# Kernel optimization log

Measured on AMD Instinct MI355X. Metric: run time of the kernel, lower is better.

## Reference

```python
import jax, jax.numpy as jnp
import numpy as np

N_HEAD = 16

def setup_inputs() -> dict:
    key = jax.random.key(0)
    ks = jax.random.split(key, 9)
    H = 2048
    def w(k, shape, scale=0.02):
        return jax.random.normal(k, shape, dtype=jnp.float32) * scale
    return {
        'h':  jax.random.normal(ks[0], (4, 2048, H), dtype=jnp.float32),
        'Wq': w(ks[1], (H, H)), 'bq': w(ks[2], (H,)),
        'Wk': w(ks[3], (H, H)), 'bk': w(ks[4], (H,)),
        'Wv': w(ks[5], (H, H)), 'bv': w(ks[6], (H,)),
        'Wo': w(ks[7], (H, H)), 'bo': w(ks[8], (H,)),
    }

def reference(h, Wq, bq, Wk, bk, Wv, bv, Wo, bo):
    B, S, H = h.shape
    nh = N_HEAD
    hd = H // nh
    # QKV projections (torch Linear: x @ W.T + b)
    q = (h @ Wq.T + bq).reshape(B, S, nh, hd)
    k = (h @ Wk.T + bk).reshape(B, S, nh, hd)
    v = (h @ Wv.T + bv).reshape(B, S, nh, hd)
    scale = 1.0 / jnp.sqrt(jnp.float32(hd))
    # causal attention scores [B, nh, S, S]
    scores = jnp.einsum('bqhd,bkhd->bhqk', q, k) * scale
    causal = jnp.tril(jnp.ones((S, S), dtype=bool))
    scores = jnp.where(causal, scores, jnp.finfo(scores.dtype).min)
    attn = jax.nn.softmax(scores, axis=-1)
    o = jnp.einsum('bhqk,bkhd->bqhd', attn, v).reshape(B, S, H)
    return o @ Wo.T + bo
```

## Files before the change

kernel.cpp:

```cpp
#include <hip/hip_runtime.h>
#include <hip/hip_bf16.h>
#include <math.h>


using bf16x8 = __attribute__((ext_vector_type(8))) __bf16;
using f32x4  = __attribute__((ext_vector_type(4))) float;
using s16x8  = __attribute__((ext_vector_type(8))) short;

#define MFMA16(a, b, c) __builtin_amdgcn_mfma_f32_16x16x32_bf16((a), (b), (c), 0, 0, 0)

__device__ __forceinline__ unsigned short f2bf(float f) {
  unsigned u = __float_as_uint(f);
  u += 0x7FFFu + ((u >> 16) & 1u);
  return (unsigned short)(u >> 16);
}

__device__ __forceinline__ void gload16(const void* g, void* l) {
  __builtin_amdgcn_global_load_lds((const __attribute__((address_space(1))) void*)g,
                                   (__attribute__((address_space(3))) void*)l,
                                   16, 0, 0);
}

__global__ void cvt_all(const float* __restrict__ h,
                        const float* __restrict__ Wq, const float* __restrict__ Wk,
                        const float* __restrict__ Wv, const float* __restrict__ Wo,
                        unsigned short* __restrict__ h_bf,
                        unsigned short* __restrict__ dqkv,
                        unsigned short* __restrict__ dwo) {
  int i = blockIdx.x * 256 + threadIdx.x;
  const float* s; unsigned short* d; int j;
  if (i < 2097152) {
    s = h; d = h_bf; j = i;
  } else {
    int w = (i - 2097152) >> 19;
    j = i & 524287;
    s = (w == 0) ? Wq : (w == 1) ? Wk : (w == 2) ? Wv : Wo;
    d = (w < 3) ? dqkv + w * 4194304 : dwo;
  }
  float4 v0 = ((const float4*)s)[2 * j];
  float4 v1 = ((const float4*)s)[2 * j + 1];
  s16x8 o;
  o[0] = (short)f2bf(v0.x); o[1] = (short)f2bf(v0.y);
  o[2] = (short)f2bf(v0.z); o[3] = (short)f2bf(v0.w);
  o[4] = (short)f2bf(v1.x); o[5] = (short)f2bf(v1.y);
  o[6] = (short)f2bf(v1.z); o[7] = (short)f2bf(v1.w);
  ((s16x8*)d)[j] = o;
}


#define GEMM_PRE()                                                             \
  const int tid = threadIdx.x;                                                 \
  const int wave = tid >> 6, lane = tid & 63;                                  \
  const int lo = lane & 15, hi = lane >> 4;                                    \
  const int wr = wave >> 2, wc = wave & 3;                                     \
  const int r4 = lane >> 2, s4 = lane & 3;                                     \
  const int scol = ((s4 ^ ((r4 >> 1) & 3)) << 3);                              \
  const unsigned short* aS[2]; const unsigned short* bS[2];                    \
  _Pragma("unroll")                                                            \
  for (int j = 0; j < 2; ++j) {                                                \
    aS[j] = A + (size_t)(m0 + (wave * 2 + j) * 16 + r4) * 2048 + scol;         \
    bS[j] = W + (size_t)(n0 + (wave * 2 + j) * 16 + r4) * 2048 + scol;         \
  }                                                                            \
  f32x4 acc[8][4] = {};

#define STAGE2(BUF, J)                                                         \
  do {                                                                         \
    gload16(aS[J], &lA[BUF][(wave * 2 + (J)) * 512]);                          \
    gload16(bS[J], &lB[BUF][(wave * 2 + (J)) * 512]);                          \
    aS[J] += 32; bS[J] += 32;                                                  \
  } while (0)

#define LDA4_(dst, MH, BUF)                                                    \
  do {                                                                         \
    _Pragma("unroll")                                                          \
    for (int im = 0; im < 4; ++im)                                             \
      dst[im] = *(const bf16x8*)&lA[BUF][(wr * 128 + (MH)*64 + im * 16 + lo) * 32 + \
                                         ((hi ^ ((lo >> 1) & 3)) << 3)];       \
  } while (0)

#define LDB4_(dst, BUF)                                                        \
  do {                                                                         \
    _Pragma("unroll")                                                          \
    for (int ni = 0; ni < 4; ++ni)                                             \
      dst[ni] = *(const bf16x8*)&lB[BUF][(wc * 64 + ni * 16 + lo) * 32 +       \
                                         ((hi ^ ((lo >> 1) & 3)) << 3)];       \
  } while (0)

#define MF16NP(MH, aF, bF)                                                     \
  do {                                                                         \
    _Pragma("unroll")                                                          \
    for (int im = 0; im < 4; ++im)                                             \
      _Pragma("unroll")                                                        \
      for (int ni = 0; ni < 4; ++ni)                                           \
        acc[(MH)*4 + im][ni] = MFMA16(aF[im], bF[ni], acc[(MH)*4 + im][ni]);   \
  } while (0)

#define BAR __builtin_amdgcn_s_barrier()
#define VMC(N) asm volatile("s_waitcnt vmcnt(" #N ")" ::: "memory")

#define TILE(RBUF, SBUF, COND, VN)                                             \
  do {                                                                         \
    bf16x8 aF[4], aG[4], bF[4];                                                \
    LDA4_(aF, 0, RBUF); LDB4_(bF, RBUF); LDA4_(aG, 1, RBUF);                   \
    if (COND) { STAGE2(SBUF, 0); STAGE2(SBUF, 1); }                            \
    __builtin_amdgcn_s_setprio(1);                                             \
    MF16NP(0, aF, bF);                                                         \
    MF16NP(1, aG, bF);                                                         \
    __builtin_amdgcn_s_setprio(0);                                             \
    VMC(VN); BAR;                                                              \
  } while (0)

#define GEMM_MAIN()                                                            \
  STAGE2(0, 0); STAGE2(0, 1); STAGE2(1, 0); STAGE2(1, 1);                      \
  STAGE2(2, 0); STAGE2(2, 1);                                                  \
  VMC(8); BAR;                                                                 \
  for (int u = 0; u < 15; ++u) {                                               \
    TILE(0, 3, true, 8); TILE(1, 0, true, 8);                                  \
    TILE(2, 1, true, 8); TILE(3, 2, true, 8);                                  \
  }                                                                            \
  TILE(0, 3, true, 8); TILE(1, 0, false, 4);                                   \
  TILE(2, 1, false, 0); TILE(3, 2, false, 0);

__global__ __launch_bounds__(512, 2)
void gemm_qkv(const unsigned short* __restrict__ A,
              const unsigned short* __restrict__ W,
              const float* __restrict__ bq, const float* __restrict__ bk,
              const float* __restrict__ bv,
              unsigned short* __restrict__ Q, unsigned short* __restrict__ Kq,
              unsigned short* __restrict__ V) {
  __shared__ unsigned short lA[4][256 * 32];
  __shared__ unsigned short lB[4][256 * 32];
  const int bid = blockIdx.x;
  const int sid = (bid & 7) * 96 + (bid >> 3);
  const int bm = sid / 24, bn = sid % 24;
  const int m0 = bm * 256, n0 = bn * 256;
  GEMM_PRE();
  GEMM_MAIN();

  const int which = n0 >> 11;
  const float* bias = (which == 0) ? bq : (which == 1) ? bk : bv;
  unsigned short* dst = (which == 0) ? Q : (which == 1) ? Kq : V;

  unsigned short* patch = (wave < 4) ? (&lA[0][0] + wave * 4608)
                                     : (&lB[0][0] + (wave - 4) * 4608);
  const int nbase = n0 + wc * 64;
  const int head = (nbase & 2047) >> 7;
  const int d0 = nbase & 127;
#pragma unroll
  for (int pass = 0; pass < 2; ++pass) {
    asm volatile("s_waitcnt lgkmcnt(0)" ::: "memory");
#pragma unroll
    for (int mi = 0; mi < 4; ++mi)
#pragma unroll
      for (int ni = 0; ni < 4; ++ni) {
        int n2 = (nbase + ni * 16 + lo) & 2047;
        float bb = bias[n2];
#pragma unroll
        for (int i = 0; i < 4; ++i)
          patch[(mi * 16 + hi * 4 + i) * 72 + ni * 16 + lo] =
              f2bf(acc[pass * 4 + mi][ni][i] + bb);
      }
    asm volatile("s_waitcnt lgkmcnt(0)" ::: "memory");
#pragma unroll
    for (int it = 0; it < 8; ++it) {
      int rl = it * 8 + (lane >> 3);
      int coff = (lane & 7) * 8;
      s16x8 v = *(const s16x8*)&patch[rl * 72 + coff];
      int m = m0 + wr * 128 + pass * 64 + rl;
      int b = m >> 11, s = m & 2047;
      *(s16x8*)&dst[(((size_t)b * 16 + head) * 2048 + s) * 128 + d0 + coff] = v;
    }
  }
}

__global__ __launch_bounds__(512, 2)
void gemm_out(const unsigned short* __restrict__ A,
              const unsigned short* __restrict__ W,
              const float* __restrict__ bo, float* __restrict__ out) {
  __shared__ unsigned short lA[4][256 * 32];
  __shared__ unsigned short lB[4][256 * 32];
  const int bid = blockIdx.x;
  const int sid = (bid & 7) * 32 + (bid >> 3);
  const int bm = sid >> 3, bn = sid & 7;
  const int m0 = bm * 256, n0 = bn * 256;
  GEMM_PRE();
  GEMM_MAIN();

  float* patch = (float*)((wave < 4) ? (&lA[0][0] + wave * 4352)
                                     : (&lB[0][0] + (wave - 4) * 4352));
  const int nbase = n0 + wc * 64;
#pragma unroll
  for (int pass = 0; pass < 4; ++pass) {
    asm volatile("s_waitcnt lgkmcnt(0)" ::: "memory");
#pragma unroll
    for (int mi = 0; mi < 2; ++mi)
#pragma unroll
      for (int ni = 0; ni < 4; ++ni) {
        float bb = bo[nbase + ni * 16 + lo];
#pragma unroll
        for (int i = 0; i < 4; ++i)
          patch[(mi * 16 + hi * 4 + i) * 68 + ni * 16 + lo] =
              acc[pass * 2 + mi][ni][i] + bb;
      }
    asm volatile("s_waitcnt lgkmcnt(0)" ::: "memory");
#pragma unroll
    for (int it = 0; it < 8; ++it) {
      int rl = it * 4 + hi;
      int coff = lo * 4;
      float4 v = *(const float4*)&patch[rl * 68 + coff];
      int m = m0 + wr * 128 + pass * 32 + rl;
      *(float4*)&out[(size_t)m * 2048 + nbase + coff] = v;
    }
  }
}

__global__ __launch_bounds__(256, 2)
void attn_kernel(const unsigned short* __restrict__ Qb,
                 const unsigned short* __restrict__ Kb,
                 const unsigned short* __restrict__ Vb,
                 unsigned short* __restrict__ Ob) {
  __shared__ unsigned short lK[2][64 * 128];
  __shared__ unsigned short lVt[144 * 72];
  __shared__ unsigned short lP[4][32 * 72];

  const int tid = threadIdx.x;
  const int wave = tid >> 6, lane = tid & 63;
  const int lo = lane & 15, hi = lane >> 4;
  const int bh = blockIdx.x & 63;
  const int pr = blockIdx.x >> 6;
  const size_t base = (size_t)bh * 2048 * 128;
  const float SCL = 0.08838834764831845f * 1.4426950408889634f;
  const float THR = 11.5416f;
  const int rr = tid & 31, c0v = (tid >> 5) * 8;

#pragma unroll
  for (int x = tid; x < 1024; x += 256)
    lVt[(128 + (x >> 6)) * 72 + (x & 63)] = 0x3F80;

#define STAGEK(KT2, BUF)                                                       \
  do {                                                                         \
    _Pragma("unroll")                                                          \
    for (int j = 0; j < 4; j++) {                                              \
      int lrow = j * 16 + wave * 4 + hi;                                       \
      int srccol = (lo * 16) ^ ((lrow & 7) << 4);                              \
      gload16(Kb + base + (size_t)((KT2) * 64 + lrow) * 128 + (srccol >> 1),   \
              &lK[BUF][(j * 16 + wave * 4) * 128]);                            \
    }                                                                          \
  } while (0)

  for (int hseq = 0; hseq < 2; ++hseq) {
    const int qt = hseq ? pr : 15 - pr;
    const int q0 = qt * 128 + wave * 32;
    const int ktn = qt * 2 + 2;
    const int qmax_w = q0 + 31;

    bf16x8 aq[2][4];
#pragma unroll
    for (int mi = 0; mi < 2; mi++)
#pragma unroll
      for (int dk = 0; dk < 4; dk++)
        aq[mi][dk] = *(const bf16x8*)&Qb[base + (size_t)(q0 + mi * 16 + lo) * 128 + dk * 32 + hi * 8];

    f32x4 acc[2][9] = {};
    float mrun[2][4];
#pragma unroll
    for (int a = 0; a < 2; a++)
#pragma unroll
      for (int b = 0; b < 4; b++) mrun[a][b] = -INFINITY;

    STAGEK(0, 0);

    for (int kt = 0; kt < ktn; kt++) {
      const unsigned short* vp0 = Vb + base + (size_t)(kt * 64 + 2 * rr) * 128 + c0v;
      s16x8 v00 = *(const s16x8*)vp0;
      s16x8 v01 = *(const s16x8*)(vp0 + 128);
      s16x8 v10 = *(const s16x8*)(vp0 + 64);
      s16x8 v11 = *(const s16x8*)(vp0 + 192);
      if (kt + 1 < ktn) { STAGEK(kt + 1, (kt + 1) & 1); VMC(8); }
      else { VMC(0); }
      BAR;

      const bool docomp = (kt * 64 <= qmax_w);
      if (docomp) {
        const unsigned short* lKc = &lK[kt & 1][0];
        f32x4 sc[2][4] = {};
        __builtin_amdgcn_s_setprio(1);
#pragma unroll
        for (int ni = 0; ni < 4; ni++)
#pragma unroll
          for (int dk = 0; dk < 4; dk++) {
            int row = ni * 16 + lo;
            int col = (dk * 32 + hi * 8) ^ ((row & 7) << 3);
            bf16x8 bk_ = *(const bf16x8*)&lKc[row * 128 + col];
            sc[0][ni] = MFMA16(aq[0][dk], bk_, sc[0][ni]);
            sc[1][ni] = MFMA16(aq[1][dk], bk_, sc[1][ni]);
          }
        __builtin_amdgcn_s_setprio(0);
        float tm[2][4];
        bool cond = true;
#pragma unroll
        for (int mi = 0; mi < 2; mi++)
#pragma unroll
          for (int i = 0; i < 4; i++) {
            int qrow = q0 + mi * 16 + hi * 4 + i;
            float mx = -INFINITY;
#pragma unroll
            for (int ni = 0; ni < 4; ni++) {
              int kc = kt * 64 + ni * 16 + lo;
              float s = sc[mi][ni][i] * SCL;
              if (kc > qrow) s = -INFINITY;
              sc[mi][ni][i] = s;
              mx = fmaxf(mx, s);
            }
            tm[mi][i] = mx;
            cond = cond && (mx <= mrun[mi][i] + THR);
          }
        if (!__all((int)cond)) {
#pragma unroll
          for (int mi = 0; mi < 2; mi++)
#pragma unroll
            for (int i = 0; i < 4; i++) {
              float mt = tm[mi][i];
              mt = fmaxf(mt, __shfl_xor(mt, 1));
              mt = fmaxf(mt, __shfl_xor(mt, 2));
              mt = fmaxf(mt, __shfl_xor(mt, 4));
              mt = fmaxf(mt, __shfl_xor(mt, 8));
              float mo = mrun[mi][i];
              float mn = fmaxf(mo, mt);
              float alpha = exp2f(mo - mn);
              mrun[mi][i] = mn;
#pragma unroll
              for (int ni = 0; ni < 9; ni++) acc[mi][ni][i] *= alpha;
            }
        }
        unsigned short* lPw = &lP[wave][0];
#pragma unroll
        for (int mi = 0; mi < 2; mi++)
#pragma unroll
          for (int i = 0; i < 4; i++) {
            float m = mrun[mi][i];
            int prow = mi * 16 + hi * 4 + i;
#pragma unroll
            for (int ni = 0; ni < 4; ni++)
              lPw[prow * 72 + ni * 16 + lo] = f2bf(exp2f(sc[mi][ni][i] - m));
          }
      }

#pragma unroll
      for (int j = 0; j < 8; j++) {
        *(ushort2*)&lVt[(c0v + j) * 72 + 2 * rr] =
            make_ushort2((unsigned short)v00[j], (unsigned short)v01[j]);
        *(ushort2*)&lVt[(c0v + 64 + j) * 72 + 2 * rr] =
            make_ushort2((unsigned short)v10[j], (unsigned short)v11[j]);
      }
      asm volatile("s_waitcnt lgkmcnt(0)" ::: "memory");
      BAR;

      if (docomp) {
        unsigned short* lPw = &lP[wave][0];
        bf16x8 ap[2][2];
#pragma unroll
        for (int mi = 0; mi < 2; mi++)
#pragma unroll
          for (int k2 = 0; k2 < 2; k2++)
            ap[mi][k2] = *(const bf16x8*)&lPw[(mi * 16 + lo) * 72 + k2 * 32 + hi * 8];
        __builtin_amdgcn_s_setprio(1);
#pragma unroll
        for (int ni = 0; ni < 9; ni++)
#pragma unroll
          for (int k2 = 0; k2 < 2; k2++) {
            bf16x8 bv_ = *(const bf16x8*)&lVt[(ni * 16 + lo) * 72 + k2 * 32 + hi * 8];
            acc[0][ni] = MFMA16(ap[0][k2], bv_, acc[0][ni]);
            acc[1][ni] = MFMA16(ap[1][k2], bv_, acc[1][ni]);
          }
        __builtin_amdgcn_s_setprio(0);
      }
    }

    const int b = bh >> 4, hh = bh & 15;
#pragma unroll
    for (int mi = 0; mi < 2; mi++)
#pragma unroll
      for (int i = 0; i < 4; i++) {
        float inv = 1.0f / acc[mi][8][i];
        int s = q0 + mi * 16 + hi * 4 + i;
        size_t rowbase = ((size_t)b * 2048 + s) * 2048 + hh * 128 + lo;
#pragma unroll
        for (int ni = 0; ni < 8; ni++)
          Ob[rowbase + ni * 16] = f2bf(acc[mi][ni][i] * inv);
      }
  }
}

extern "C" void kernel_launch(void* const* d_in, const int* in_sizes, int n_in,
                              void* d_out, int out_size, void* d_ws, size_t ws_size,
                              hipStream_t stream) {
  const float* h  = (const float*)d_in[0];
  const float* Wq = (const float*)d_in[1];
  const float* bq = (const float*)d_in[2];
  const float* Wk = (const float*)d_in[3];
  const float* bk = (const float*)d_in[4];
  const float* Wv = (const float*)d_in[5];
  const float* bv = (const float*)d_in[6];
  const float* Wo = (const float*)d_in[7];
  const float* bo = (const float*)d_in[8];
  float* out = (float*)d_out;

  char* ws = (char*)d_ws;
  unsigned short* h_bf  = (unsigned short*)(ws + 0);
  unsigned short* Qb    = (unsigned short*)(ws + 33554432);
  unsigned short* Kb    = (unsigned short*)(ws + 67108864);
  unsigned short* Vb    = (unsigned short*)(ws + 100663296);
  unsigned short* Wqkv  = (unsigned short*)(ws + 134217728);
  unsigned short* Wo_bf = (unsigned short*)(ws + 159383552);
  unsigned short* Ob    = h_bf;

  cvt_all<<<16384, 256, 0, stream>>>(h, Wq, Wk, Wv, Wo, h_bf, Wqkv, Wo_bf);

  gemm_qkv<<<dim3(768), dim3(512), 0, stream>>>(h_bf, Wqkv, bq, bk, bv, Qb, Kb, Vb);

  attn_kernel<<<dim3(512), dim3(256), 0, stream>>>(Qb, Kb, Vb, Ob);

  gemm_out<<<dim3(256), dim3(512), 0, stream>>>(Ob, Wo_bf, bo, out);
}
```

Measured before the change: 420.4 us.

## Shrink GEMM tiles to 256x128 with triple-buffered LDS for higher occupancy

Both projection GEMMs move from 256x256 to 256x128 output tiles and from a 4-deep to a 3-deep LDS ring, which cuts shared memory per block. Launch bounds rise to 4 blocks per CU and grid sizes double. The point is better occupancy and wave count: gemm_out now has 512 blocks instead of 256 on a 256-CU part. The cost is lower arithmetic intensity per tile and more global traffic for A, plus fewer accumulator registers per wave, so the 4-block bound may or may not be met.

```diff
diff --git a/kernel.cpp b/kernel.cpp
--- a/kernel.cpp
+++ b/kernel.cpp
@@ -55,35 +55,33 @@
   const int wr = wave >> 2, wc = wave & 3;                                     \
   const int r4 = lane >> 2, s4 = lane & 3;                                     \
   const int scol = ((s4 ^ ((r4 >> 1) & 3)) << 3);                              \
-  const unsigned short* aS[2]; const unsigned short* bS[2];                    \
+  const int swz = ((hi ^ ((lo >> 1) & 3)) << 3);                               \
+  const unsigned short* aS[2]; const unsigned short* bS;                       \
   _Pragma("unroll")                                                            \
-  for (int j = 0; j < 2; ++j) {                                                \
+  for (int j = 0; j < 2; ++j)                                                  \
     aS[j] = A + (size_t)(m0 + (wave * 2 + j) * 16 + r4) * 2048 + scol;         \
-    bS[j] = W + (size_t)(n0 + (wave * 2 + j) * 16 + r4) * 2048 + scol;         \
-  }                                                                            \
-  f32x4 acc[8][4] = {};
-
-#define STAGE2(BUF, J)                                                         \
-  do {                                                                         \
-    gload16(aS[J], &lA[BUF][(wave * 2 + (J)) * 512]);                          \
-    gload16(bS[J], &lB[BUF][(wave * 2 + (J)) * 512]);                          \
-    aS[J] += 32; bS[J] += 32;                                                  \
+  bS = W + (size_t)(n0 + wave * 16 + r4) * 2048 + scol;                        \
+  f32x4 acc[8][2] = {};
+
+#define STAGE3(BUF)                                                            \
+  do {                                                                         \
+    gload16(aS[0], &lA[BUF][(wave * 2 + 0) * 512]); aS[0] += 32;               \
+    gload16(aS[1], &lA[BUF][(wave * 2 + 1) * 512]); aS[1] += 32;               \
+    gload16(bS, &lB[BUF][wave * 512]); bS += 32;                               \
   } while (0)
 
 #define LDA4_(dst, MH, BUF)                                                    \
   do {                                                                         \
     _Pragma("unroll")                                                          \
     for (int im = 0; im < 4; ++im)                                             \
-      dst[im] = *(const bf16x8*)&lA[BUF][(wr * 128 + (MH)*64 + im * 16 + lo) * 32 + \
-                                         ((hi ^ ((lo >> 1) & 3)) << 3)];       \
-  } while (0)
-
-#define LDB4_(dst, BUF)                                                        \
+      dst[im] = *(const bf16x8*)&lA[BUF][(wr * 128 + (MH)*64 + im * 16 + lo) * 32 + swz]; \
+  } while (0)
+
+#define LDB2_(dst, BUF)                                                        \
   do {                                                                         \
     _Pragma("unroll")                                                          \
-    for (int ni = 0; ni < 4; ++ni)                                             \
-      dst[ni] = *(const bf16x8*)&lB[BUF][(wc * 64 + ni * 16 + lo) * 32 +       \
-                                         ((hi ^ ((lo >> 1) & 3)) << 3)];       \
+    for (int ni = 0; ni < 2; ++ni)                                             \
+      dst[ni] = *(const bf16x8*)&lB[BUF][(wc * 32 + ni * 16 + lo) * 32 + swz]; \
   } while (0)
 
 #define MF16NP(MH, aF, bF)                                                     \
@@ -91,7 +89,7 @@
     _Pragma("unroll")                                                          \
     for (int im = 0; im < 4; ++im)                                             \
       _Pragma("unroll")                                                        \
-      for (int ni = 0; ni < 4; ++ni)                                           \
+      for (int ni = 0; ni < 2; ++ni)                                           \
         acc[(MH)*4 + im][ni] = MFMA16(aF[im], bF[ni], acc[(MH)*4 + im][ni]);   \
   } while (0)
 
@@ -100,9 +98,9 @@
 
 #define TILE(RBUF, SBUF, COND, VN)                                             \
   do {                                                                         \
-    bf16x8 aF[4], aG[4], bF[4];                                                \
-    LDA4_(aF, 0, RBUF); LDB4_(bF, RBUF); LDA4_(aG, 1, RBUF);                   \
-    if (COND) { STAGE2(SBUF, 0); STAGE2(SBUF, 1); }                            \
+    bf16x8 aF[4], aG[4], bF[2];                                                \
+    LDA4_(aF, 0, RBUF); LDB2_(bF, RBUF); LDA4_(aG, 1, RBUF);                   \
+    if (COND) STAGE3(SBUF);                                                    \
     __builtin_amdgcn_s_setprio(1);                                             \
     MF16NP(0, aF, bF);                                                         \
     MF16NP(1, aG, bF);                                                         \
@@ -111,29 +109,27 @@
   } while (0)
 
 #define GEMM_MAIN()                                                            \
-  STAGE2(0, 0); STAGE2(0, 1); STAGE2(1, 0); STAGE2(1, 1);                      \
-  STAGE2(2, 0); STAGE2(2, 1);                                                  \
-  VMC(8); BAR;                                                                 \
-  for (int u = 0; u < 15; ++u) {                                               \
-    TILE(0, 3, true, 8); TILE(1, 0, true, 8);                                  \
-    TILE(2, 1, true, 8); TILE(3, 2, true, 8);                                  \
+  STAGE3(0); STAGE3(1);                                                        \
+  VMC(3); BAR;                                                                 \
+  for (int u = 0; u < 20; ++u) {                                               \
+    TILE(0, 2, true, 3); TILE(1, 0, true, 3); TILE(2, 1, true, 3);             \
   }                                                                            \
-  TILE(0, 3, true, 8); TILE(1, 0, false, 4);                                   \
-  TILE(2, 1, false, 0); TILE(3, 2, false, 0);
-
-__global__ __launch_bounds__(512, 2)
+  TILE(0, 2, true, 3); TILE(1, 0, true, 3);                                    \
+  TILE(2, 1, false, 0); TILE(0, 0, false, 0);
+
+__global__ __launch_bounds__(512, 4)
 void gemm_qkv(const unsigned short* __restrict__ A,
               const unsigned short* __restrict__ W,
               const float* __restrict__ bq, const float* __restrict__ bk,
               const float* __restrict__ bv,
               unsigned short* __restrict__ Q, unsigned short* __restrict__ Kq,
               unsigned short* __restrict__ V) {
-  __shared__ unsigned short lA[4][256 * 32];
-  __shared__ unsigned short lB[4][256 * 32];
+  __shared__ unsigned short lA[3][256 * 32];
+  __shared__ unsigned short lB[3][128 * 32];
   const int bid = blockIdx.x;
-  const int sid = (bid & 7) * 96 + (bid >> 3);
-  const int bm = sid / 24, bn = sid % 24;
-  const int m0 = bm * 256, n0 = bn * 256;
+  const int sid = (bid & 7) * 192 + (bid >> 3);
+  const int bm = sid / 48, bn = sid % 48;
+  const int m0 = bm * 256, n0 = bn * 128;
   GEMM_PRE();
   GEMM_MAIN();
 
@@ -141,31 +137,30 @@
   const float* bias = (which == 0) ? bq : (which == 1) ? bk : bv;
   unsigned short* dst = (which == 0) ? Q : (which == 1) ? Kq : V;
 
-  unsigned short* patch = (wave < 4) ? (&lA[0][0] + wave * 4608)
-                                     : (&lB[0][0] + (wave - 4) * 4608);
-  const int nbase = n0 + wc * 64;
+  unsigned short* patch = &lA[0][0] + wave * 2560;
+  const int nbase = n0 + wc * 32;
   const int head = (nbase & 2047) >> 7;
   const int d0 = nbase & 127;
+  float bb[2];
+#pragma unroll
+  for (int ni = 0; ni < 2; ++ni) bb[ni] = bias[(nbase + ni * 16 + lo) & 2047];
 #pragma unroll
   for (int pass = 0; pass < 2; ++pass) {
     asm volatile("s_waitcnt lgkmcnt(0)" ::: "memory");
 #pragma unroll
     for (int mi = 0; mi < 4; ++mi)
 #pragma unroll
-      for (int ni = 0; ni < 4; ++ni) {
-        int n2 = (nbase + ni * 16 + lo) & 2047;
-        float bb = bias[n2];
+      for (int ni = 0; ni < 2; ++ni)
 #pragma unroll
         for (int i = 0; i < 4; ++i)
-          patch[(mi * 16 + hi * 4 + i) * 72 + ni * 16 + lo] =
-              f2bf(acc[pass * 4 + mi][ni][i] + bb);
-      }
+          patch[(mi * 16 + hi * 4 + i) * 40 + ni * 16 + lo] =
+              f2bf(acc[pass * 4 + mi][ni][i] + bb[ni]);
     asm volatile("s_waitcnt lgkmcnt(0)" ::: "memory");
 #pragma unroll
-    for (int it = 0; it < 8; ++it) {
-      int rl = it * 8 + (lane >> 3);
-      int coff = (lane & 7) * 8;
-      s16x8 v = *(const s16x8*)&patch[rl * 72 + coff];
+    for (int it = 0; it < 4; ++it) {
+      int rl = it * 16 + (lane >> 2);
+      int coff = (lane & 3) * 8;
+      s16x8 v = *(const s16x8*)&patch[rl * 40 + coff];
       int m = m0 + wr * 128 + pass * 64 + rl;
       int b = m >> 11, s = m & 2047;
       *(s16x8*)&dst[(((size_t)b * 16 + head) * 2048 + s) * 128 + d0 + coff] = v;
@@ -173,41 +168,41 @@
   }
 }
 
-__global__ __launch_bounds__(512, 2)
+__global__ __launch_bounds__(512, 4)
 void gemm_out(const unsigned short* __restrict__ A,
               const unsigned short* __restrict__ W,
               const float* __restrict__ bo, float* __restrict__ out) {
-  __shared__ unsigned short lA[4][256 * 32];
-  __shared__ unsigned short lB[4][256 * 32];
+  __shared__ unsigned short lA[3][256 * 32];
+  __shared__ unsigned short lB[3][128 * 32];
   const int bid = blockIdx.x;
-  const int sid = (bid & 7) * 32 + (bid >> 3);
-  const int bm = sid >> 3, bn = sid & 7;
-  const int m0 = bm * 256, n0 = bn * 256;
+  const int sid = (bid & 7) * 64 + (bid >> 3);
+  const int bm = sid >> 4, bn = sid & 15;
+  const int m0 = bm * 256, n0 = bn * 128;
   GEMM_PRE();
   GEMM_MAIN();
 
-  float* patch = (float*)((wave < 4) ? (&lA[0][0] + wave * 4352)
-                                     : (&lB[0][0] + (wave - 4) * 4352));
-  const int nbase = n0 + wc * 64;
+  float* patch = (float*)(&lA[0][0]) + wave * 1152;
+  const int nbase = n0 + wc * 32;
+  float bb[2];
+#pragma unroll
+  for (int ni = 0; ni < 2; ++ni) bb[ni] = bo[nbase + ni * 16 + lo];
 #pragma unroll
   for (int pass = 0; pass < 4; ++pass) {
     asm volatile("s_waitcnt lgkmcnt(0)" ::: "memory");
 #pragma unroll
     for (int mi = 0; mi < 2; ++mi)
 #pragma unroll
-      for (int ni = 0; ni < 4; ++ni) {
-        float bb = bo[nbase + ni * 16 + lo];
+      for (int ni = 0; ni < 2; ++ni)
 #pragma unroll
         for (int i = 0; i < 4; ++i)
-          patch[(mi * 16 + hi * 4 + i) * 68 + ni * 16 + lo] =
-              acc[pass * 2 + mi][ni][i] + bb;
-      }
+          patch[(mi * 16 + hi * 4 + i) * 36 + ni * 16 + lo] =
+              acc[pass * 2 + mi][ni][i] + bb[ni];
     asm volatile("s_waitcnt lgkmcnt(0)" ::: "memory");
 #pragma unroll
-    for (int it = 0; it < 8; ++it) {
-      int rl = it * 4 + hi;
-      int coff = lo * 4;
-      float4 v = *(const float4*)&patch[rl * 68 + coff];
+    for (int it = 0; it < 4; ++it) {
+      int rl = it * 8 + (lane >> 3);
+      int coff = (lane & 7) * 4;
+      float4 v = *(const float4*)&patch[rl * 36 + coff];
       int m = m0 + wr * 128 + pass * 32 + rl;
       *(float4*)&out[(size_t)m * 2048 + nbase + coff] = v;
     }
@@ -417,9 +412,9 @@
 
   cvt_all<<<16384, 256, 0, stream>>>(h, Wq, Wk, Wv, Wo, h_bf, Wqkv, Wo_bf);
 
-  gemm_qkv<<<dim3(768), dim3(512), 0, stream>>>(h_bf, Wqkv, bq, bk, bv, Qb, Kb, Vb);
+  gemm_qkv<<<dim3(1536), dim3(512), 0, stream>>>(h_bf, Wqkv, bq, bk, bv, Qb, Kb, Vb);
 
   attn_kernel<<<dim3(512), dim3(256), 0, stream>>>(Qb, Kb, Vb, Ob);
 
-  gemm_out<<<dim3(256), dim3(512), 0, stream>>>(Ob, Wo_bf, bo, out);
-}
+  gemm_out<<<dim3(512), dim3(512), 0, stream>>>(Ob, Wo_bf, bo, out);
+}
```

After: 459.7 us. 9.3% more time.

## Restructure GEMM main loop into finer-grained A/B staged ping-pong windows

Applied to the files above, without the earlier changes.

Replaces the 4-buffer, one-tile-per-barrier GEMM pipeline with a 2x2 LDS layout. Each 128-wide K window is split into eight half-tile MFMA phases separated by barriers. Global-to-LDS loads for A and B are issued separately and interleaved with the phases, which aims to overlap memory traffic with MFMA work at finer granularity. In exchange there are many more barriers per K step, and the waitcnt accounting must stay correct.

```diff
diff --git a/kernel.cpp b/kernel.cpp
--- a/kernel.cpp
+++ b/kernel.cpp
@@ -55,71 +55,104 @@
   const int wr = wave >> 2, wc = wave & 3;                                     \
   const int r4 = lane >> 2, s4 = lane & 3;                                     \
   const int scol = ((s4 ^ ((r4 >> 1) & 3)) << 3);                              \
-  const unsigned short* aS[2]; const unsigned short* bS[2];                    \
+  const int swz = ((hi ^ ((lo >> 1) & 3)) << 3);                               \
+  const unsigned short* aBase[2]; const unsigned short* bBase[2];              \
   _Pragma("unroll")                                                            \
   for (int j = 0; j < 2; ++j) {                                                \
-    aS[j] = A + (size_t)(m0 + (wave * 2 + j) * 16 + r4) * 2048 + scol;         \
-    bS[j] = W + (size_t)(n0 + (wave * 2 + j) * 16 + r4) * 2048 + scol;         \
+    aBase[j] = A + (size_t)(m0 + (wave * 2 + j) * 16 + r4) * 2048 + scol;      \
+    bBase[j] = W + (size_t)(n0 + (wave * 2 + j) * 16 + r4) * 2048 + scol;      \
   }                                                                            \
   f32x4 acc[8][4] = {};
 
-#define STAGE2(BUF, J)                                                         \
-  do {                                                                         \
-    gload16(aS[J], &lA[BUF][(wave * 2 + (J)) * 512]);                          \
-    gload16(bS[J], &lB[BUF][(wave * 2 + (J)) * 512]);                          \
-    aS[J] += 32; bS[J] += 32;                                                  \
-  } while (0)
-
-#define LDA4_(dst, MH, BUF)                                                    \
+#define STAGEA(D, KK, KOFF)                                                    \
+  do {                                                                         \
+    gload16(aBase[0] + (KOFF), &lA[D][KK][(wave * 2 + 0) * 512]);              \
+    gload16(aBase[1] + (KOFF), &lA[D][KK][(wave * 2 + 1) * 512]);              \
+  } while (0)
+
+#define STAGEB(D, KK, KOFF)                                                    \
+  do {                                                                         \
+    gload16(bBase[0] + (KOFF), &lB[D][KK][(wave * 2 + 0) * 512]);              \
+    gload16(bBase[1] + (KOFF), &lB[D][KK][(wave * 2 + 1) * 512]);              \
+  } while (0)
+
+#define LDA4W(dst, D, KK, MH)                                                  \
   do {                                                                         \
     _Pragma("unroll")                                                          \
     for (int im = 0; im < 4; ++im)                                             \
-      dst[im] = *(const bf16x8*)&lA[BUF][(wr * 128 + (MH)*64 + im * 16 + lo) * 32 + \
-                                         ((hi ^ ((lo >> 1) & 3)) << 3)];       \
-  } while (0)
-
-#define LDB4_(dst, BUF)                                                        \
+      dst[im] = *(const bf16x8*)&lA[D][KK][(wr * 128 + (MH)*64 + im * 16 + lo) * 32 + swz]; \
+  } while (0)
+
+#define LDB4W(dst, D, KK)                                                      \
   do {                                                                         \
     _Pragma("unroll")                                                          \
     for (int ni = 0; ni < 4; ++ni)                                             \
-      dst[ni] = *(const bf16x8*)&lB[BUF][(wc * 64 + ni * 16 + lo) * 32 +       \
-                                         ((hi ^ ((lo >> 1) & 3)) << 3)];       \
-  } while (0)
-
-#define MF16NP(MH, aF, bF)                                                     \
-  do {                                                                         \
+      dst[ni] = *(const bf16x8*)&lB[D][KK][(wc * 64 + ni * 16 + lo) * 32 + swz]; \
+  } while (0)
+
+#define MFP(MH, aF, bF)                                                        \
+  do {                                                                         \
+    __builtin_amdgcn_s_setprio(1);                                             \
     _Pragma("unroll")                                                          \
     for (int im = 0; im < 4; ++im)                                             \
       _Pragma("unroll")                                                        \
       for (int ni = 0; ni < 4; ++ni)                                           \
         acc[(MH)*4 + im][ni] = MFMA16(aF[im], bF[ni], acc[(MH)*4 + im][ni]);   \
+    __builtin_amdgcn_s_setprio(0);                                             \
   } while (0)
 
 #define BAR __builtin_amdgcn_s_barrier()
 #define VMC(N) asm volatile("s_waitcnt vmcnt(" #N ")" ::: "memory")
 
-#define TILE(RBUF, SBUF, COND, VN)                                             \
-  do {                                                                         \
-    bf16x8 aF[4], aG[4], bF[4];                                                \
-    LDA4_(aF, 0, RBUF); LDB4_(bF, RBUF); LDA4_(aG, 1, RBUF);                   \
-    if (COND) { STAGE2(SBUF, 0); STAGE2(SBUF, 1); }                            \
-    __builtin_amdgcn_s_setprio(1);                                             \
-    MF16NP(0, aF, bF);                                                         \
-    MF16NP(1, aG, bF);                                                         \
-    __builtin_amdgcn_s_setprio(0);                                             \
-    VMC(VN); BAR;                                                              \
+#define WINDOW(KB, CS, V2, V4, V6, V8)                                         \
+  do {                                                                         \
+    bf16x8 aF[4], bF[4];                                                       \
+                                \
+    LDA4W(aF, 0, 0, 0); LDB4W(bF, 0, 0);                                       \
+    STAGEA(1, 1, (KB) + 96);                                                   \
+    BAR; MFP(0, aF, bF); BAR;                                                  \
+                                \
+    LDA4W(aF, 0, 0, 1);                                                        \
+    if (CS) STAGEB(0, 0, (KB) + 128);                                          \
+    BAR; MFP(1, aF, bF); VMC(V2); BAR;                                         \
+                                          \
+    LDA4W(aF, 0, 1, 0); LDB4W(bF, 0, 1);                                       \
+    if (CS) STAGEA(0, 0, (KB) + 128);                                          \
+    BAR; MFP(0, aF, bF); BAR;                                                  \
+                                          \
+    LDA4W(aF, 0, 1, 1);                                                        \
+    if (CS) STAGEB(0, 1, (KB) + 160);                                          \
+    BAR; MFP(1, aF, bF); VMC(V4); BAR;                                         \
+                                          \
+    LDA4W(aF, 1, 0, 0); LDB4W(bF, 1, 0);                                       \
+    if (CS) STAGEA(0, 1, (KB) + 160);                                          \
+    BAR; MFP(0, aF, bF); BAR;                                                  \
+                                \
+    LDA4W(aF, 1, 0, 1);                                                        \
+    if (CS) STAGEB(1, 0, (KB) + 192);                                          \
+    BAR; MFP(1, aF, bF); VMC(V6); BAR;                                         \
+                                          \
+    LDA4W(aF, 1, 1, 0); LDB4W(bF, 1, 1);                                       \
+    if (CS) STAGEA(1, 0, (KB) + 192);                                          \
+    BAR; MFP(0, aF, bF); BAR;                                                  \
+                                          \
+    LDA4W(aF, 1, 1, 1);                                                        \
+    if (CS) STAGEB(1, 1, (KB) + 224);                                          \
+    BAR; MFP(1, aF, bF); VMC(V8); BAR;                                         \
   } while (0)
 
 #define GEMM_MAIN()                                                            \
-  STAGE2(0, 0); STAGE2(0, 1); STAGE2(1, 0); STAGE2(1, 1);                      \
-  STAGE2(2, 0); STAGE2(2, 1);                                                  \
+                 \
+  STAGEB(0, 0, 0);  STAGEA(0, 0, 0);                                           \
+  STAGEB(0, 1, 32); STAGEA(0, 1, 32);                                          \
+  STAGEB(1, 0, 64); STAGEA(1, 0, 64);                                          \
+  STAGEB(1, 1, 96);                                                            \
   VMC(8); BAR;                                                                 \
   for (int u = 0; u < 15; ++u) {                                               \
-    TILE(0, 3, true, 8); TILE(1, 0, true, 8);                                  \
-    TILE(2, 1, true, 8); TILE(3, 2, true, 8);                                  \
+    const int kb = u * 128;                                                    \
+    WINDOW(kb, true, 8, 8, 8, 8);                                              \
   }                                                                            \
-  TILE(0, 3, true, 8); TILE(1, 0, false, 4);                                   \
-  TILE(2, 1, false, 0); TILE(3, 2, false, 0);
+  WINDOW(1920, false, 8, 4, 0, 0);
 
 __global__ __launch_bounds__(512, 2)
 void gemm_qkv(const unsigned short* __restrict__ A,
@@ -128,8 +161,8 @@
               const float* __restrict__ bv,
               unsigned short* __restrict__ Q, unsigned short* __restrict__ Kq,
               unsigned short* __restrict__ V) {
-  __shared__ unsigned short lA[4][256 * 32];
-  __shared__ unsigned short lB[4][256 * 32];
+  __shared__ unsigned short lA[2][2][256 * 32];
+  __shared__ unsigned short lB[2][2][256 * 32];
   const int bid = blockIdx.x;
   const int sid = (bid & 7) * 96 + (bid >> 3);
   const int bm = sid / 24, bn = sid % 24;
@@ -141,8 +174,8 @@
   const float* bias = (which == 0) ? bq : (which == 1) ? bk : bv;
   unsigned short* dst = (which == 0) ? Q : (which == 1) ? Kq : V;
 
-  unsigned short* patch = (wave < 4) ? (&lA[0][0] + wave * 4608)
-                                     : (&lB[0][0] + (wave - 4) * 4608);
+  unsigned short* patch = (wave < 4) ? (&lA[0][0][0] + wave * 4608)
+                                     : (&lB[0][0][0] + (wave - 4) * 4608);
   const int nbase = n0 + wc * 64;
   const int head = (nbase & 2047) >> 7;
   const int d0 = nbase & 127;
@@ -177,8 +210,8 @@
 void gemm_out(const unsigned short* __restrict__ A,
               const unsigned short* __restrict__ W,
               const float* __restrict__ bo, float* __restrict__ out) {
-  __shared__ unsigned short lA[4][256 * 32];
-  __shared__ unsigned short lB[4][256 * 32];
+  __shared__ unsigned short lA[2][2][256 * 32];
+  __shared__ unsigned short lB[2][2][256 * 32];
   const int bid = blockIdx.x;
   const int sid = (bid & 7) * 32 + (bid >> 3);
   const int bm = sid >> 3, bn = sid & 7;
@@ -186,8 +219,8 @@
   GEMM_PRE();
   GEMM_MAIN();
 
-  float* patch = (float*)((wave < 4) ? (&lA[0][0] + wave * 4352)
-                                     : (&lB[0][0] + (wave - 4) * 4352));
+  float* patch = (float*)((wave < 4) ? (&lA[0][0][0] + wave * 4352)
+                                     : (&lB[0][0][0] + (wave - 4) * 4352));
   const int nbase = n0 + wc * 64;
 #pragma unroll
   for (int pass = 0; pass < 4; ++pass) {
```

Measured after the change: 453.5 us. 1.08x slower.
